# Performance work log

Measured on AMD Instinct MI355X. Metric: run time of the kernel, lower is better.

The kernel has to match this reference:

```python
import jax, jax.numpy as jnp
import numpy as np
import math

N_HEAD = 16
N_KV_HEAD = 4
HEAD_DIM = 128
ROTARY_DIM = 128
ROTARY_BASE = 10000
N_CTX = 2048


def _sin_cos(rotary_dim, n_ctx, base):
    pos = np.arange(n_ctx, dtype=np.float32)
    dim = np.arange(rotary_dim // 2, dtype=np.float32)
    freq = base ** (dim / (rotary_dim / 2))
    freq = np.concatenate([freq, freq])  # non-adjacent-pairs layout
    angles = pos[:, None] / freq[None, :]
    return jnp.asarray(np.sin(angles)), jnp.asarray(np.cos(angles))


def _rotate_half(x):
    n = x.shape[-1] // 2
    return jnp.concatenate([-x[..., n:], x[..., :n]], axis=-1)


def setup_inputs() -> dict:
    key = jax.random.key(0)
    ks = jax.random.split(key, 5)
    B, T, C = 2, 2048, 2048
    kv = N_KV_HEAD * HEAD_DIM
    s = 0.02
    return {
        "x": jax.random.normal(ks[0], (B, T, C), jnp.float32),
        "Wq": jax.random.normal(ks[1], (C, C), jnp.float32) * s,
        "Wk": jax.random.normal(ks[2], (kv, C), jnp.float32) * s,
        "Wv": jax.random.normal(ks[3], (kv, C), jnp.float32) * s,
        "Wo": jax.random.normal(ks[4], (C, C), jnp.float32) * s,
    }


def reference(x, Wq, Wk, Wv, Wo):
    B, T, C = x.shape
    q = (x @ Wq.T).reshape(B, T, N_HEAD, HEAD_DIM).transpose(0, 2, 1, 3)    # bhtd
    k = (x @ Wk.T).reshape(B, T, N_KV_HEAD, HEAD_DIM).transpose(0, 2, 1, 3)
    v = (x @ Wv.T).reshape(B, T, N_KV_HEAD, HEAD_DIM).transpose(0, 2, 1, 3)

    sin, cos = _sin_cos(ROTARY_DIM, N_CTX, ROTARY_BASE)
    pos = jnp.arange(T)
    c = cos[pos][None, None, :, :]  # 1,1,T,rot
    s = sin[pos][None, None, :, :]
    q = q * c + _rotate_half(q) * s
    k = k * c + _rotate_half(k) * s

    rep = N_HEAD // N_KV_HEAD
    k = jnp.repeat(k, rep, axis=1)
    v = jnp.repeat(v, rep, axis=1)

    scale = 1.0 / math.sqrt(HEAD_DIM)
    att = jnp.einsum("bhqd,bhkd->bhqk", q, k) * scale
    causal = jnp.tril(jnp.ones((T, T), bool))
    att = jnp.where(causal[None, None], att, -jnp.inf)
    att = jax.nn.softmax(att, axis=-1)
    y = jnp.einsum("bhqk,bhkd->bhqd", att, v)
    y = y.transpose(0, 2, 1, 3).reshape(B, T, C)
    return y @ Wo.T
```

## Files before the change

kernel.cpp:

```cpp
#include <hip/hip_runtime.h>
#include <hip/hip_bf16.h>

typedef float f32x4 __attribute__((ext_vector_type(4)));
typedef short s16x8 __attribute__((ext_vector_type(8)));
typedef short s16x4 __attribute__((ext_vector_type(4)));

__device__ __forceinline__ short f2bf(float f) {
  union { float f; unsigned u; } v; v.f = f;
  unsigned r = v.u + 0x7fffu + ((v.u >> 16) & 1u);
  return (short)(r >> 16);
}
__device__ __forceinline__ float bf2f(short s) {
  union { unsigned u; float f; } v; v.u = ((unsigned)(unsigned short)s) << 16;
  return v.f;
}

__device__ __forceinline__ void gload_lds16(const short* g, short* l) {
  __builtin_amdgcn_global_load_lds(
      (const __attribute__((address_space(1))) void*)g,
      (__attribute__((address_space(3))) void*)l, 16, 0, 0);
}

__global__ __launch_bounds__(256) void k_f2bf(const float* __restrict__ in,
                                              short* __restrict__ out, int n8) {
  int i = blockIdx.x * 256 + threadIdx.x;
  if (i >= n8) return;
  const float4* p = (const float4*)in + (size_t)i * 2;
  float4 a = p[0], b = p[1];
  s16x8 o;
  o[0] = f2bf(a.x); o[1] = f2bf(a.y); o[2] = f2bf(a.z); o[3] = f2bf(a.w);
  o[4] = f2bf(b.x); o[5] = f2bf(b.y); o[6] = f2bf(b.z); o[7] = f2bf(b.w);
  *(s16x8*)(out + (size_t)i * 8) = o;
}

template <int MODE>
__global__ __launch_bounds__(256) void k_gemm_bt(const short* __restrict__ A,
                                                 const short* __restrict__ Bw,
                                                 void* __restrict__ C,
                                                 void* __restrict__ C2,
                                                 void* __restrict__ C3,
                                                 int M, int N, int K) {
  __shared__ __align__(16) short As[128 * 64];
  __shared__ __align__(16) short Bs[128 * 64];
  const int tid = threadIdx.x;
  const int w = tid >> 6, lane = tid & 63;
  const int wm = w >> 1, wn = w & 1;
  const int bm = blockIdx.y, bn = blockIdx.x;
  const int l15 = lane & 15, l4 = lane >> 4;

  f32x4 acc[4][4] = {};

  const int nk = K >> 6;
  for (int kt = 0; kt < nk; ++kt) {
    __syncthreads();
#pragma unroll
    for (int it = 0; it < 4; ++it) {
      int p = it * 256 + tid;
      int p0 = it * 256 + w * 64;
      int r = p >> 3, j = p & 7;
      int jsrc = j ^ (r & 7);
      gload_lds16(A + (size_t)(bm * 128 + r) * K + kt * 64 + jsrc * 8, &As[p0 * 8]);
      gload_lds16(Bw + (size_t)(bn * 128 + r) * K + kt * 64 + jsrc * 8, &Bs[p0 * 8]);
    }
    __syncthreads();
#pragma unroll
    for (int kk = 0; kk < 2; ++kk) {
      s16x8 af[4], bf[4];
      const int jj = kk * 4 + l4;
#pragma unroll
      for (int mi = 0; mi < 4; ++mi) {
        int r = wm * 64 + mi * 16 + l15;
        af[mi] = *(const s16x8*)&As[(r * 8 + (jj ^ (r & 7))) * 8];
      }
#pragma unroll
      for (int ni = 0; ni < 4; ++ni) {
        int r = wn * 64 + ni * 16 + l15;
        bf[ni] = *(const s16x8*)&Bs[(r * 8 + (jj ^ (r & 7))) * 8];
      }
      __builtin_amdgcn_s_setprio(1);
#pragma unroll
      for (int mi = 0; mi < 4; ++mi)
#pragma unroll
        for (int ni = 0; ni < 4; ++ni)
          acc[mi][ni] = __builtin_amdgcn_mfma_f32_16x16x32_bf16(
              af[mi], bf[ni], acc[mi][ni], 0, 0, 0);
      __builtin_amdgcn_s_setprio(0);
    }
  }

#pragma unroll
  for (int mi = 0; mi < 4; ++mi) {
#pragma unroll
    for (int ni = 0; ni < 4; ++ni) {
      int row0 = bm * 128 + wm * 64 + mi * 16 + l4 * 4;
      int col = bn * 128 + wn * 64 + ni * 16 + l15;
      if (MODE == 1) {
        float* Cf = (float*)C;
#pragma unroll
        for (int r2 = 0; r2 < 4; ++r2)
          Cf[(size_t)(row0 + r2) * N + col] = acc[mi][ni][r2];
      } else {
        if (col < 2048) {
          short* Qo = (short*)C;
#pragma unroll
          for (int r2 = 0; r2 < 4; ++r2)
            Qo[(size_t)(row0 + r2) * 2048 + col] = f2bf(acc[mi][ni][r2]);
        } else if (col < 2560) {
          short* Ko = (short*)C2;
#pragma unroll
          for (int r2 = 0; r2 < 4; ++r2)
            Ko[(size_t)(row0 + r2) * 512 + (col - 2048)] = f2bf(acc[mi][ni][r2]);
        } else {
          short* Vo = (short*)C3;
          int b = row0 >> 11, t0 = row0 & 2047;
          s16x4 pk;
#pragma unroll
          for (int r2 = 0; r2 < 4; ++r2) pk[r2] = f2bf(acc[mi][ni][r2]);
          *(s16x4*)&Vo[(size_t)b * 1048576 + (size_t)(col - 2560) * 2048 + t0] = pk;
        }
      }
    }
  }
}

__global__ __launch_bounds__(256) void k_rope(short* __restrict__ X, int shift,
                                              int rowstride, float mul) {
  int idx = blockIdx.x * 256 + threadIdx.x;
  int row = idx >> shift;
  int rem = idx & ((1 << shift) - 1);
  int h = rem >> 6, d = rem & 63;
  int t = row & 2047;
  float inv = exp2f(-(float)d * (13.287712379549449f / 64.f));
  float ang = (float)t * inv;
  float s, c;
  sincosf(ang, &s, &c);
  size_t base = (size_t)row * rowstride + h * 128 + d;
  float q0 = bf2f(X[base]), q1 = bf2f(X[base + 64]);
  X[base] = f2bf((q0 * c - q1 * s) * mul);
  X[base + 64] = f2bf((q1 * c + q0 * s) * mul);
}

__device__ __forceinline__ void attn_tile(const s16x8* qf, const short* Ksb,
                                          const short* Vsb, short* P,
                                          f32x4* acc, float* m, float* lsum,
                                          bool diag, int rt0, int l15, int l4) {
  f32x4 s[4] = {};
  __builtin_amdgcn_s_setprio(1);
#pragma unroll
  for (int kk = 0; kk < 4; ++kk) {
    const int jj = kk * 4 + l4;
#pragma unroll
    for (int jt = 0; jt < 4; ++jt) {
      int r = jt * 16 + l15;
      s16x8 kf = *(const s16x8*)&Ksb[(r * 16 + (jj ^ (r & 7))) * 8];
      s[jt] = __builtin_amdgcn_mfma_f32_16x16x32_bf16(qf[kk], kf, s[jt], 0, 0, 0);
    }
  }
  __builtin_amdgcn_s_setprio(0);

  float alpha[4];
#pragma unroll
  for (int r = 0; r < 4; ++r) {
    if (diag) {
#pragma unroll
      for (int jt = 0; jt < 4; ++jt)
        if (jt * 16 + l15 > rt0 + r) s[jt][r] = -1e30f;
    }
    float mr = fmaxf(fmaxf(s[0][r], s[1][r]), fmaxf(s[2][r], s[3][r]));
#pragma unroll
    for (int mk = 1; mk < 16; mk <<= 1) mr = fmaxf(mr, __shfl_xor(mr, mk));
    float mnew = fmaxf(m[r], mr);
    alpha[r] = exp2f(m[r] - mnew);
    m[r] = mnew;
    float rs = 0.f;
#pragma unroll
    for (int jt = 0; jt < 4; ++jt) {
      float p = exp2f(s[jt][r] - mnew);
      s[jt][r] = p;
      rs += p;
    }
#pragma unroll
    for (int mk = 1; mk < 16; mk <<= 1) rs += __shfl_xor(rs, mk);
    lsum[r] = lsum[r] * alpha[r] + rs;
  }

#pragma unroll
  for (int nt = 0; nt < 8; ++nt)
#pragma unroll
    for (int r = 0; r < 4; ++r) acc[nt][r] *= alpha[r];

#pragma unroll
  for (int jt = 0; jt < 4; ++jt)
#pragma unroll
    for (int r = 0; r < 4; ++r)
      P[(l4 * 4 + r) * 80 + jt * 16 + l15] = f2bf(s[jt][r]);

#pragma unroll
  for (int kk2 = 0; kk2 < 2; ++kk2) {
    s16x8 pf = *(const s16x8*)&P[l15 * 80 + kk2 * 32 + l4 * 8];
    const int jj = kk2 * 4 + l4;
    __builtin_amdgcn_s_setprio(1);
#pragma unroll
    for (int nt = 0; nt < 8; ++nt) {
      int r = nt * 16 + l15;
      s16x8 vf = *(const s16x8*)&Vsb[(r * 8 + (jj ^ (r & 7))) * 8];
      acc[nt] = __builtin_amdgcn_mfma_f32_16x16x32_bf16(pf, vf, acc[nt], 0, 0, 0);
    }
    __builtin_amdgcn_s_setprio(0);
  }
}

__global__ __launch_bounds__(256, 2) void k_attn2(const short* __restrict__ Q,
                                                  const short* __restrict__ Kb,
                                                  const short* __restrict__ Vt,
                                                  short* __restrict__ Y) {
  __shared__ __align__(16) short Ks[2][64 * 128];
  __shared__ __align__(16) short Vs[2][128 * 64];
  __shared__ __align__(16) short Pb[4][16 * 80];

  const int tid = threadIdx.x;
  const int w = tid >> 6, lane = tid & 63;
  const int l15 = lane & 15, l4 = lane >> 4;
  const int pair = blockIdx.x, h = blockIdx.y, b = blockIdx.z;
  const int kh = h >> 2;
  const int qtA = pair, qtB = 31 - pair;

  s16x8 qfA[4], qfB[4];
  {
    const size_t rowA = (size_t)(b * 2048 + qtA * 64 + w * 16 + l15);
    const size_t rowB = (size_t)(b * 2048 + qtB * 64 + w * 16 + l15);
#pragma unroll
    for (int kk = 0; kk < 4; ++kk) {
      qfA[kk] = *(const s16x8*)(Q + rowA * 2048 + h * 128 + kk * 32 + l4 * 8);
      qfB[kk] = *(const s16x8*)(Q + rowB * 2048 + h * 128 + kk * 32 + l4 * 8);
    }
  }

  f32x4 accA[8] = {}, accB[8] = {};
  float mA[4], mB[4], lA[4], lB[4];
#pragma unroll
  for (int r = 0; r < 4; ++r) {
    mA[r] = -1e30f; mB[r] = -1e30f; lA[r] = 0.f; lB[r] = 0.f;
  }

  auto stage = [&](int buf, int j) {
    const int kv0 = j * 64;
#pragma unroll
    for (int it = 0; it < 4; ++it) {
      int p = it * 256 + tid;
      int p0 = it * 256 + w * 64;
      int r = p >> 4, jc = p & 15;
      int jsrc = jc ^ (r & 7);
      gload_lds16(Kb + (size_t)(b * 2048 + kv0 + r) * 512 + kh * 128 + jsrc * 8,
                  &Ks[buf][p0 * 8]);
    }
#pragma unroll
    for (int it = 0; it < 4; ++it) {
      int p = it * 256 + tid;
      int p0 = it * 256 + w * 64;
      int r = p >> 3, jc = p & 7;
      int jsrc = jc ^ (r & 7);
      gload_lds16(Vt + (size_t)b * 1048576 + (size_t)(kh * 128 + r) * 2048 +
                      kv0 + jsrc * 8,
                  &Vs[buf][p0 * 8]);
    }
  };

  const int rt0 = w * 16 + l4 * 4;
  const int nt = qtB + 1;

  stage(0, 0);
  __syncthreads();

  for (int j = 0; j < nt; ++j) {
    const int cur = j & 1;
    if (j + 1 < nt) stage(cur ^ 1, j + 1);
    attn_tile(qfB, &Ks[cur][0], &Vs[cur][0], &Pb[w][0], accB, mB, lB,
              j == qtB, rt0, l15, l4);
    if (j <= qtA)
      attn_tile(qfA, &Ks[cur][0], &Vs[cur][0], &Pb[w][0], accA, mA, lA,
                j == qtA, rt0, l15, l4);
    __syncthreads();
  }

#pragma unroll
  for (int ntd = 0; ntd < 8; ++ntd) {
#pragma unroll
    for (int r = 0; r < 4; ++r) {
      size_t rA = (size_t)(b * 2048 + qtA * 64 + rt0 + r);
      size_t rB = (size_t)(b * 2048 + qtB * 64 + rt0 + r);
      Y[rA * 2048 + h * 128 + ntd * 16 + l15] = f2bf(accA[ntd][r] / lA[r]);
      Y[rB * 2048 + h * 128 + ntd * 16 + l15] = f2bf(accB[ntd][r] / lB[r]);
    }
  }
}

extern "C" void kernel_launch(void* const* d_in, const int* in_sizes, int n_in,
                              void* d_out, int out_size, void* d_ws, size_t ws_size,
                              hipStream_t stream) {
  (void)in_sizes; (void)n_in; (void)out_size; (void)ws_size;
  const float* x  = (const float*)d_in[0];
  const float* Wq = (const float*)d_in[1];
  const float* Wk = (const float*)d_in[2];
  const float* Wv = (const float*)d_in[3];
  const float* Wo = (const float*)d_in[4];

  char* ws = (char*)d_ws;
  short* xb    = (short*)(ws);
  short* wqkvb = (short*)(ws + 16777216);
  short* wob   = (short*)(ws + 29360128);
  short* Qb    = (short*)(ws + 37748736);
  short* Kb    = (short*)(ws + 54525952);
  short* Vtb   = (short*)(ws + 58720256);
  short* Yb    = (short*)(ws + 62914560);

  k_f2bf<<<4096, 256, 0, stream>>>(x, xb, 1048576);
  k_f2bf<<<2048, 256, 0, stream>>>(Wq, wqkvb, 524288);
  k_f2bf<<<512, 256, 0, stream>>>(Wk, wqkvb + 4194304, 131072);
  k_f2bf<<<512, 256, 0, stream>>>(Wv, wqkvb + 5242880, 131072);
  k_f2bf<<<2048, 256, 0, stream>>>(Wo, wob, 524288);

  k_gemm_bt<3><<<dim3(24, 32), 256, 0, stream>>>(xb, wqkvb, Qb, Kb, Vtb,
                                                 4096, 3072, 2048);

  k_rope<<<16384, 256, 0, stream>>>(Qb, 10, 2048, 0.12751758912141852f);
  k_rope<<<4096, 256, 0, stream>>>(Kb, 8, 512, 1.0f);

  k_attn2<<<dim3(16, 16, 2), 256, 0, stream>>>(Qb, Kb, Vtb, Yb);

  k_gemm_bt<1><<<dim3(16, 32), 256, 0, stream>>>(Yb, wob, d_out, nullptr,
                                                 nullptr, 4096, 2048, 2048);
}
```

Baseline: 236.1 us.

## Rewrite attention with 32x32 MFMA, register-resident P, lazy rescale

```diff
diff --git a/kernel.cpp b/kernel.cpp
--- a/kernel.cpp
+++ b/kernel.cpp
@@ -2,6 +2,7 @@
 #include <hip/hip_bf16.h>
 
 typedef float f32x4 __attribute__((ext_vector_type(4)));
+typedef float f32x16 __attribute__((ext_vector_type(16)));
 typedef short s16x8 __attribute__((ext_vector_type(8)));
 typedef short s16x4 __attribute__((ext_vector_type(4)));
 
@@ -13,6 +14,11 @@
 __device__ __forceinline__ float bf2f(short s) {
   union { unsigned u; float f; } v; v.u = ((unsigned)(unsigned short)s) << 16;
   return v.f;
+}
+__device__ __forceinline__ unsigned cvtpk(float lo, float hi) {
+  unsigned r;
+  asm("v_cvt_pk_bf16_f32 %0, %1, %2" : "=v"(r) : "v"(lo), "v"(hi));
+  return r;
 }
 
 __device__ __forceinline__ void gload_lds16(const short* g, short* l) {
@@ -140,157 +146,179 @@
   X[base + 64] = f2bf((q1 * c + q0 * s) * mul);
 }
 
-__device__ __forceinline__ void attn_tile(const s16x8* qf, const short* Ksb,
-                                          const short* Vsb, short* P,
-                                          f32x4* acc, float* m, float* lsum,
-                                          bool diag, int rt0, int l15, int l4) {
-  f32x4 s[4] = {};
-  __builtin_amdgcn_s_setprio(1);
-#pragma unroll
-  for (int kk = 0; kk < 4; ++kk) {
-    const int jj = kk * 4 + l4;
-#pragma unroll
-    for (int jt = 0; jt < 4; ++jt) {
-      int r = jt * 16 + l15;
-      s16x8 kf = *(const s16x8*)&Ksb[(r * 16 + (jj ^ (r & 7))) * 8];
-      s[jt] = __builtin_amdgcn_mfma_f32_16x16x32_bf16(qf[kk], kf, s[jt], 0, 0, 0);
-    }
-  }
-  __builtin_amdgcn_s_setprio(0);
-
-  float alpha[4];
-#pragma unroll
-  for (int r = 0; r < 4; ++r) {
-    if (diag) {
-#pragma unroll
-      for (int jt = 0; jt < 4; ++jt)
-        if (jt * 16 + l15 > rt0 + r) s[jt][r] = -1e30f;
-    }
-    float mr = fmaxf(fmaxf(s[0][r], s[1][r]), fmaxf(s[2][r], s[3][r]));
-#pragma unroll
-    for (int mk = 1; mk < 16; mk <<= 1) mr = fmaxf(mr, __shfl_xor(mr, mk));
-    float mnew = fmaxf(m[r], mr);
-    alpha[r] = exp2f(m[r] - mnew);
-    m[r] = mnew;
-    float rs = 0.f;
-#pragma unroll
-    for (int jt = 0; jt < 4; ++jt) {
-      float p = exp2f(s[jt][r] - mnew);
-      s[jt][r] = p;
-      rs += p;
-    }
-#pragma unroll
-    for (int mk = 1; mk < 16; mk <<= 1) rs += __shfl_xor(rs, mk);
-    lsum[r] = lsum[r] * alpha[r] + rs;
-  }
-
-#pragma unroll
-  for (int nt = 0; nt < 8; ++nt)
-#pragma unroll
-    for (int r = 0; r < 4; ++r) acc[nt][r] *= alpha[r];
-
-#pragma unroll
-  for (int jt = 0; jt < 4; ++jt)
-#pragma unroll
-    for (int r = 0; r < 4; ++r)
-      P[(l4 * 4 + r) * 80 + jt * 16 + l15] = f2bf(s[jt][r]);
-
-#pragma unroll
-  for (int kk2 = 0; kk2 < 2; ++kk2) {
-    s16x8 pf = *(const s16x8*)&P[l15 * 80 + kk2 * 32 + l4 * 8];
-    const int jj = kk2 * 4 + l4;
-    __builtin_amdgcn_s_setprio(1);
-#pragma unroll
-    for (int nt = 0; nt < 8; ++nt) {
-      int r = nt * 16 + l15;
-      s16x8 vf = *(const s16x8*)&Vsb[(r * 8 + (jj ^ (r & 7))) * 8];
-      acc[nt] = __builtin_amdgcn_mfma_f32_16x16x32_bf16(pf, vf, acc[nt], 0, 0, 0);
-    }
-    __builtin_amdgcn_s_setprio(0);
-  }
-}
-
-__global__ __launch_bounds__(256, 2) void k_attn2(const short* __restrict__ Q,
+__global__ __launch_bounds__(256, 2) void k_attn3(const short* __restrict__ Q,
                                                   const short* __restrict__ Kb,
                                                   const short* __restrict__ Vt,
                                                   short* __restrict__ Y) {
   __shared__ __align__(16) short Ks[2][64 * 128];
   __shared__ __align__(16) short Vs[2][128 * 64];
-  __shared__ __align__(16) short Pb[4][16 * 80];
 
   const int tid = threadIdx.x;
   const int w = tid >> 6, lane = tid & 63;
-  const int l15 = lane & 15, l4 = lane >> 4;
-  const int pair = blockIdx.x, h = blockIdx.y, b = blockIdx.z;
+  const int l31 = lane & 31, h5 = lane >> 5;
+  const int qx = blockIdx.x, h = blockIdx.y, b = blockIdx.z;
+  const int qi = b ? (15 - qx) : qx;
   const int kh = h >> 2;
-  const int qtA = pair, qtB = 31 - pair;
-
-  s16x8 qfA[4], qfB[4];
-  {
-    const size_t rowA = (size_t)(b * 2048 + qtA * 64 + w * 16 + l15);
-    const size_t rowB = (size_t)(b * 2048 + qtB * 64 + w * 16 + l15);
-#pragma unroll
-    for (int kk = 0; kk < 4; ++kk) {
-      qfA[kk] = *(const s16x8*)(Q + rowA * 2048 + h * 128 + kk * 32 + l4 * 8);
-      qfB[kk] = *(const s16x8*)(Q + rowB * 2048 + h * 128 + kk * 32 + l4 * 8);
-    }
-  }
-
-  f32x4 accA[8] = {}, accB[8] = {};
-  float mA[4], mB[4], lA[4], lB[4];
-#pragma unroll
-  for (int r = 0; r < 4; ++r) {
-    mA[r] = -1e30f; mB[r] = -1e30f; lA[r] = 0.f; lB[r] = 0.f;
-  }
+
+  s16x8 qf[8];
+  const int qrow_local = qi * 128 + w * 32 + l31;
+  const size_t qrow = (size_t)(b * 2048 + qrow_local);
+#pragma unroll
+  for (int f = 0; f < 8; ++f)
+    qf[f] = *(const s16x8*)(Q + qrow * 2048 + h * 128 + f * 16 + h5 * 8);
+
+  f32x16 oacc[4] = {};
+  float m = -1e30f, l = 0.f;
+
+  const int jmax = 2 * qi + 1;
 
   auto stage = [&](int buf, int j) {
-    const int kv0 = j * 64;
 #pragma unroll
     for (int it = 0; it < 4; ++it) {
       int p = it * 256 + tid;
       int p0 = it * 256 + w * 64;
-      int r = p >> 4, jc = p & 15;
-      int jsrc = jc ^ (r & 7);
-      gload_lds16(Kb + (size_t)(b * 2048 + kv0 + r) * 512 + kh * 128 + jsrc * 8,
+      int r = p >> 4, c = p & 15;
+      int csrc = (c - r) & 15;
+      gload_lds16(Kb + (size_t)(b * 2048 + j * 64 + r) * 512 + kh * 128 + csrc * 8,
                   &Ks[buf][p0 * 8]);
     }
 #pragma unroll
     for (int it = 0; it < 4; ++it) {
       int p = it * 256 + tid;
       int p0 = it * 256 + w * 64;
-      int r = p >> 3, jc = p & 7;
-      int jsrc = jc ^ (r & 7);
+      int r = p >> 3, c = p & 7;
+      int csrc = (c - r) & 7;
       gload_lds16(Vt + (size_t)b * 1048576 + (size_t)(kh * 128 + r) * 2048 +
-                      kv0 + jsrc * 8,
+                      j * 64 + csrc * 8,
                   &Vs[buf][p0 * 8]);
     }
   };
-
-  const int rt0 = w * 16 + l4 * 4;
-  const int nt = qtB + 1;
 
   stage(0, 0);
   __syncthreads();
 
-  for (int j = 0; j < nt; ++j) {
+  for (int j = 0; j <= jmax; ++j) {
     const int cur = j & 1;
-    if (j + 1 < nt) stage(cur ^ 1, j + 1);
-    attn_tile(qfB, &Ks[cur][0], &Vs[cur][0], &Pb[w][0], accB, mB, lB,
-              j == qtB, rt0, l15, l4);
-    if (j <= qtA)
-      attn_tile(qfA, &Ks[cur][0], &Vs[cur][0], &Pb[w][0], accA, mA, lA,
-                j == qtA, rt0, l15, l4);
+    if (j < jmax) stage(cur ^ 1, j + 1);
+
+    f32x16 sa0 = {}, sa1 = {};
+    __builtin_amdgcn_s_setprio(1);
+#pragma unroll
+    for (int f = 0; f < 8; ++f) {
+      int c = f * 2 + h5;
+      int r0 = l31, r1 = 32 + l31;
+      s16x8 k0 = *(const s16x8*)&Ks[cur][(r0 * 16 + ((c + r0) & 15)) * 8];
+      s16x8 k1 = *(const s16x8*)&Ks[cur][(r1 * 16 + ((c + r1) & 15)) * 8];
+      sa0 = __builtin_amdgcn_mfma_f32_32x32x16_bf16(k0, qf[f], sa0, 0, 0, 0);
+      sa1 = __builtin_amdgcn_mfma_f32_32x32x16_bf16(k1, qf[f], sa1, 0, 0, 0);
+    }
+    __builtin_amdgcn_s_setprio(0);
+
+    if (j >= 2 * qi) {
+      const int kv0 = j * 64;
+#pragma unroll
+      for (int rg = 0; rg < 16; ++rg) {
+        int krow = (rg & 3) + 8 * (rg >> 2) + 4 * h5;
+        if (kv0 + krow > qrow_local) sa0[rg] = -3.0e38f;
+        if (kv0 + 32 + krow > qrow_local) sa1[rg] = -3.0e38f;
+      }
+    }
+
+    float mx[16];
+#pragma unroll
+    for (int i = 0; i < 16; ++i) mx[i] = fmaxf(sa0[i], sa1[i]);
+#pragma unroll
+    for (int stp = 8; stp > 0; stp >>= 1)
+#pragma unroll
+      for (int i = 0; i < stp; ++i) mx[i] = fmaxf(mx[i], mx[i + stp]);
+    float pm = fmaxf(mx[0], __shfl_xor(mx[0], 32));
+
+    if (!__all(pm - m <= 8.f)) {
+      float mn = fmaxf(m, pm);
+      float al = exp2f(m - mn);
+      m = mn;
+      l *= al;
+#pragma unroll
+      for (int d = 0; d < 4; ++d)
+#pragma unroll
+        for (int i = 0; i < 16; ++i) oacc[d][i] *= al;
+    }
+
+    float sm[16];
+#pragma unroll
+    for (int i = 0; i < 16; ++i) {
+      float e0 = exp2f(sa0[i] - m);
+      float e1 = exp2f(sa1[i] - m);
+      sa0[i] = e0; sa1[i] = e1;
+      sm[i] = e0 + e1;
+    }
+#pragma unroll
+    for (int stp = 8; stp > 0; stp >>= 1)
+#pragma unroll
+      for (int i = 0; i < stp; ++i) sm[i] += sm[i + stp];
+    l += sm[0] + __shfl_xor(sm[0], 32);
+
+    unsigned u0[8], u1[8];
+#pragma unroll
+    for (int g = 0; g < 4; ++g) {
+      u0[2 * g]     = cvtpk(sa0[4 * g + 0], sa0[4 * g + 1]);
+      u0[2 * g + 1] = cvtpk(sa0[4 * g + 2], sa0[4 * g + 3]);
+      u1[2 * g]     = cvtpk(sa1[4 * g + 0], sa1[4 * g + 1]);
+      u1[2 * g + 1] = cvtpk(sa1[4 * g + 2], sa1[4 * g + 3]);
+    }
+    unsigned pu0[8], pu1[8];
+#pragma unroll
+    for (int g2 = 0; g2 < 8; ++g2) {
+      pu0[g2] = __shfl_xor(u0[g2], 32);
+      pu1[g2] = __shfl_xor(u1[g2], 32);
+    }
+    s16x8 pb[4];
+#pragma unroll
+    for (int fp = 0; fp < 4; ++fp) {
+      int j0a = (4 * fp) & 6, j0b = (4 * fp + 2) & 6;
+      union { unsigned uu[4]; s16x8 v; } cv;
+      if (fp < 2) {
+        cv.uu[0] = h5 ? pu0[j0b]     : u0[j0a];
+        cv.uu[1] = h5 ? pu0[j0b + 1] : u0[j0a + 1];
+        cv.uu[2] = h5 ? u0[j0b]      : pu0[j0a];
+        cv.uu[3] = h5 ? u0[j0b + 1]  : pu0[j0a + 1];
+      } else {
+        cv.uu[0] = h5 ? pu1[j0b]     : u1[j0a];
+        cv.uu[1] = h5 ? pu1[j0b + 1] : u1[j0a + 1];
+        cv.uu[2] = h5 ? u1[j0b]      : pu1[j0a];
+        cv.uu[3] = h5 ? u1[j0b + 1]  : pu1[j0a + 1];
+      }
+      pb[fp] = cv.v;
+    }
+
+    __builtin_amdgcn_s_setprio(1);
+#pragma unroll
+    for (int dblk = 0; dblk < 4; ++dblk) {
+#pragma unroll
+      for (int fp = 0; fp < 4; ++fp) {
+        int r = dblk * 32 + l31;
+        int slot = (fp * 2 + h5 + r) & 7;
+        s16x8 vf = *(const s16x8*)&Vs[cur][(r * 8 + slot) * 8];
+        oacc[dblk] = __builtin_amdgcn_mfma_f32_32x32x16_bf16(vf, pb[fp],
+                                                             oacc[dblk], 0, 0, 0);
+      }
+    }
+    __builtin_amdgcn_s_setprio(0);
+
     __syncthreads();
   }
 
-#pragma unroll
-  for (int ntd = 0; ntd < 8; ++ntd) {
-#pragma unroll
-    for (int r = 0; r < 4; ++r) {
-      size_t rA = (size_t)(b * 2048 + qtA * 64 + rt0 + r);
-      size_t rB = (size_t)(b * 2048 + qtB * 64 + rt0 + r);
-      Y[rA * 2048 + h * 128 + ntd * 16 + l15] = f2bf(accA[ntd][r] / lA[r]);
-      Y[rB * 2048 + h * 128 + ntd * 16 + l15] = f2bf(accB[ntd][r] / lB[r]);
+  float inv = 1.f / l;
+#pragma unroll
+  for (int dblk = 0; dblk < 4; ++dblk) {
+#pragma unroll
+    for (int rg = 0; rg < 4; ++rg) {
+      unsigned lo = cvtpk(oacc[dblk][4 * rg + 0] * inv, oacc[dblk][4 * rg + 1] * inv);
+      unsigned hi = cvtpk(oacc[dblk][4 * rg + 2] * inv, oacc[dblk][4 * rg + 3] * inv);
+      int d0 = dblk * 32 + 8 * rg + 4 * h5;
+      uint2 st;
+      st.x = lo; st.y = hi;
+      *(uint2*)(Y + qrow * 2048 + h * 128 + d0) = st;
     }
   }
 }
@@ -326,7 +354,7 @@
   k_rope<<<16384, 256, 0, stream>>>(Qb, 10, 2048, 0.12751758912141852f);
   k_rope<<<4096, 256, 0, stream>>>(Kb, 8, 512, 1.0f);
 
-  k_attn2<<<dim3(16, 16, 2), 256, 0, stream>>>(Qb, Kb, Vtb, Yb);
+  k_attn3<<<dim3(16, 16, 2), 256, 0, stream>>>(Qb, Kb, Vtb, Yb);
 
   k_gemm_bt<1><<<dim3(16, 32), 256, 0, stream>>>(Yb, wob, d_out, nullptr,
                                                  nullptr, 4096, 2048, 2048);
```

Result: faster. 211.2 us (-10.5%).
